# Kernel optimization log

Hardware: AMD Instinct MI355X
Metric: run time of the kernel (lower is better)

The kernel has to match this reference:

```python
import jax, jax.numpy as jnp
import numpy as np

B, SEQ, FEAT, OUT = 8192, 128, 16, 512
D = SEQ * FEAT  # 2048 flattened input dim
H1, H2 = 128, 64


def setup_inputs() -> dict:
    key = jax.random.key(0)
    ks = jax.random.split(key, 9)
    def lin(k, fan_in, shape):
        bound = 1.0 / np.sqrt(fan_in)
        return jax.random.uniform(k, shape, jnp.float32, -bound, bound)
    return {
        "x": jax.random.normal(ks[0], (B, SEQ, FEAT), jnp.float32),
        "W1": lin(ks[1], D, (H1, D)),  "b1": lin(ks[2], D, (H1,)),
        "W2": lin(ks[3], H1, (H2, H1)), "b2": lin(ks[4], H1, (H2,)),
        "W3": lin(ks[5], H2, (D, H2)),  "b3": lin(ks[6], H2, (D,)),
        "Wp": lin(ks[7], D, (OUT, D)),  "bp": lin(ks[8], D, (OUT,)),
    }


def reference(x, W1, b1, W2, b2, W3, b3, Wp, bp):
    # Flatten: [B, D]
    xf = x.reshape(x.shape[0], -1)
    # Forward through base MLP (dropout = identity in eval) to get ReLU masks.
    h1 = xf @ W1.T + b1            # [B, H1]
    m1 = (h1 > 0).astype(xf.dtype)
    h2 = (h1 * m1) @ W2.T + b2     # [B, H2]
    m2 = (h2 > 0).astype(xf.dtype)
    # Per-sample Jacobian of base_forward: J = W3 diag(m2) W2 diag(m1) W1  [D, D]
    # v = (J - J^T) @ 1 = J @ 1 - J^T @ 1 ; both are cheap chained matvecs.
    w1_rows = W1.sum(axis=1)       # W1 @ 1_D, [H1]
    row = ((m1 * w1_rows) @ W2.T * m2) @ W3.T        # J @ 1, [B, D]
    w3_cols = W3.sum(axis=0)       # W3^T @ 1_D, [H2]
    col = ((m2 * w3_cols) @ W2 * m1) @ W1            # J^T @ 1, [B, D]
    v = row - col                  # antisymmetrized row-sum, [B, D]
    return v @ Wp.T + bp           # [B, OUT]
```

## Files before the change

### kernel.cpp

```cpp
#include <hip/hip_runtime.h>


#define B_N   8192
#define D_N   2048
#define H1_N  128
#define H2_N  64
#define OUT_N 512

#define WS_W1R  0
#define WS_W3C  128
#define WS_W2T  256
#define WS_WPC  16384
#define WS_WPCP 114688
#define WS_H1PA 131072
#define WS_H1PB 1179648
#define WS_AT   2228224

__global__ __launch_bounds__(256) void k_pre(const float* __restrict__ W1,
                                             const float* __restrict__ W2,
                                             const float* __restrict__ W3,
                                             float* __restrict__ ws) {
  int b = blockIdx.x, t = threadIdx.x;
  __shared__ float red[256];
  if (b < 128) {
    float s = 0.f;
    const float* row = W1 + (size_t)b * D_N;
    for (int i = t; i < D_N; i += 256) s += row[i];
    red[t] = s; __syncthreads();
    for (int off = 128; off > 0; off >>= 1) { if (t < off) red[t] += red[t + off]; __syncthreads(); }
    if (t == 0) ws[WS_W1R + b] = red[0];
  } else if (b < 192) {
    int c = b - 128;
    float s = 0.f;
    for (int d = t; d < D_N; d += 256) s += W3[(size_t)d * H2_N + c];
    red[t] = s; __syncthreads();
    for (int off = 128; off > 0; off >>= 1) { if (t < off) red[t] += red[t + off]; __syncthreads(); }
    if (t == 0) ws[WS_W3C + c] = red[0];
  } else {
    int flat = (b - 192) * 256 + t;
    int j = flat >> 6, u = flat & 63;
    ws[WS_W2T + j * H2_N + u] = W2[u * H1_N + j];
  }
}

__global__ __launch_bounds__(128) void k_wpc(const float* __restrict__ W1,
                                             const float* __restrict__ W3,
                                             const float* __restrict__ Wp,
                                             float* __restrict__ ws) {
  int b = blockIdx.x, t = threadIdx.x;
  int rt = b % 6, ot = (b / 6) % 8, kc = b / 48;
  __shared__ float As[32 * 68];
  __shared__ float Bs[64 * 68];
  int rg = t >> 4, og = t & 15;
  float acc[4][4];
  #pragma unroll
  for (int i = 0; i < 4; ++i)
    #pragma unroll
    for (int j = 0; j < 4; ++j) acc[i][j] = 0.f;
  for (int sub = 0; sub < 4; ++sub) {
    int k0 = kc * 256 + sub * 64;
    __syncthreads();
    if (rt < 2) {
      #pragma unroll
      for (int i = 0; i < 4; ++i) {
        int flat = i * 128 + t;
        int rq = flat & 7, kl = flat >> 3;
        const float4 v = *reinterpret_cast<const float4*>(W3 + (size_t)(k0 + kl) * H2_N + rt * 32 + rq * 4);
        As[(rq * 4 + 0) * 68 + kl] = v.x;
        As[(rq * 4 + 1) * 68 + kl] = v.y;
        As[(rq * 4 + 2) * 68 + kl] = v.z;
        As[(rq * 4 + 3) * 68 + kl] = v.w;
      }
    } else {
      #pragma unroll
      for (int i = 0; i < 4; ++i) {
        int flat = i * 128 + t;
        int kq = flat & 15, rl = flat >> 4;
        const float4 v = *reinterpret_cast<const float4*>(W1 + (size_t)(rt * 32 + rl - 64) * D_N + k0 + kq * 4);
        *reinterpret_cast<float4*>(&As[rl * 68 + kq * 4]) = v;
      }
    }
    #pragma unroll
    for (int i = 0; i < 8; ++i) {
      int flat = i * 128 + t;
      int kq = flat & 15, ol = flat >> 4;
      const float4 v = *reinterpret_cast<const float4*>(Wp + (size_t)(ot * 64 + ol) * D_N + k0 + kq * 4);
      *reinterpret_cast<float4*>(&Bs[ol * 68 + kq * 4]) = v;
    }
    __syncthreads();
    for (int k = 0; k < 64; k += 4) {
      float4 a[4], bb[4];
      #pragma unroll
      for (int i = 0; i < 4; ++i) a[i] = *reinterpret_cast<const float4*>(&As[(rg * 4 + i) * 68 + k]);
      #pragma unroll
      for (int j = 0; j < 4; ++j) bb[j] = *reinterpret_cast<const float4*>(&Bs[(og * 4 + j) * 68 + k]);
      #pragma unroll
      for (int i = 0; i < 4; ++i)
        #pragma unroll
        for (int j = 0; j < 4; ++j) {
          acc[i][j] = fmaf(a[i].x, bb[j].x, acc[i][j]);
          acc[i][j] = fmaf(a[i].y, bb[j].y, acc[i][j]);
          acc[i][j] = fmaf(a[i].z, bb[j].z, acc[i][j]);
          acc[i][j] = fmaf(a[i].w, bb[j].w, acc[i][j]);
        }
    }
  }
  float* P = ws + WS_WPCP + (size_t)kc * (192 * 512);
  #pragma unroll
  for (int i = 0; i < 4; ++i) {
    int r = rt * 32 + rg * 4 + i;
    #pragma unroll
    for (int j = 0; j < 4; ++j)
      P[r * 512 + ot * 64 + og * 4 + j] = acc[i][j];
  }
}

__global__ __launch_bounds__(256) void k_wpc_red(float* __restrict__ ws) {
  int idx = (blockIdx.x * 256 + threadIdx.x) * 4;
  float4 s = make_float4(0.f, 0.f, 0.f, 0.f);
  #pragma unroll
  for (int p = 0; p < 8; ++p) {
    const float4 v = *reinterpret_cast<const float4*>(ws + WS_WPCP + (size_t)p * (192 * 512) + idx);
    s.x += v.x; s.y += v.y; s.z += v.z; s.w += v.w;
  }
  *reinterpret_cast<float4*>(ws + WS_WPC + idx) = s;
}

__global__ __launch_bounds__(128) void k_h1(const float* __restrict__ x,
                                            const float* __restrict__ W1,
                                            float* __restrict__ ws) {
  __shared__ float xs[64 * 65];
  int b = blockIdx.x;
  int st = b >> 3, ut = (b >> 1) & 3, kh = b & 1;
  int s0 = st * 64;
  int t = threadIdx.x;
  int lane = t & 63;
  int wv = __builtin_amdgcn_readfirstlane(t >> 6);
  int u0 = ut * 32 + wv * 16;
  float acc[16];
  #pragma unroll
  for (int i = 0; i < 16; ++i) acc[i] = 0.f;
  for (int cc = 0; cc < 16; ++cc) {
    int kc = kh * 1024 + cc * 64;
    __syncthreads();
    #pragma unroll
    for (int r = 0; r < 8; ++r) {
      int flat = r * 128 + t;
      int kq = flat & 15;
      int s  = flat >> 4;
      const float4 v = *reinterpret_cast<const float4*>(x + (size_t)(s0 + s) * D_N + kc + kq * 4);
      xs[(kq * 4 + 0) * 65 + s] = v.x;
      xs[(kq * 4 + 1) * 65 + s] = v.y;
      xs[(kq * 4 + 2) * 65 + s] = v.z;
      xs[(kq * 4 + 3) * 65 + s] = v.w;
    }
    __syncthreads();
    const float* wbase = W1 + (size_t)u0 * D_N + kc;
    for (int k4 = 0; k4 < 64; k4 += 4) {
      float a0 = xs[(k4 + 0) * 65 + lane];
      float a1 = xs[(k4 + 1) * 65 + lane];
      float a2 = xs[(k4 + 2) * 65 + lane];
      float a3 = xs[(k4 + 3) * 65 + lane];
      #pragma unroll
      for (int uu = 0; uu < 16; ++uu) {
        const float* wr = wbase + (size_t)uu * D_N + k4;
        float c = acc[uu];
        c = fmaf(wr[0], a0, c);
        c = fmaf(wr[1], a1, c);
        c = fmaf(wr[2], a2, c);
        c = fmaf(wr[3], a3, c);
        acc[uu] = c;
      }
    }
  }
  float* hp = ws + (kh ? WS_H1PB : WS_H1PA);
  #pragma unroll
  for (int uu = 0; uu < 16; ++uu)
    hp[(size_t)(u0 + uu) * B_N + s0 + lane] = acc[uu];
}

__global__ __launch_bounds__(512) void k_mid(const float* __restrict__ b1,
                                             const float* __restrict__ b2,
                                             const float* __restrict__ W2,
                                             float* __restrict__ ws) {
  __shared__ float hs[128 * 65];
  __shared__ float sb[64 * 65];
  int s0 = blockIdx.x * 64;
  int t = threadIdx.x;
  int lane = t & 63;
  int wv = __builtin_amdgcn_readfirstlane(t >> 6);
  const float* PA = ws + WS_H1PA;
  const float* PB = ws + WS_H1PB;
  const float* W2T = ws + WS_W2T;
  const float* w1r = ws + WS_W1R;
  const float* w3c = ws + WS_W3C;
  float* A_T = ws + WS_AT;
  #pragma unroll
  for (int jj = 0; jj < 16; ++jj) {
    int j = wv * 16 + jj;
    hs[j * 65 + lane] = PA[(size_t)j * B_N + s0 + lane]
                      + PB[(size_t)j * B_N + s0 + lane] + b1[j];
  }
  __syncthreads();
  {
    int u0 = wv * 8;
    float h2a[8], ta[8];
    #pragma unroll
    for (int i = 0; i < 8; ++i) { h2a[i] = b2[u0 + i]; ta[i] = 0.f; }
    for (int j = 0; j < H1_N; ++j) {
      float h = hs[j * 65 + lane];
      float g = fmaxf(h, 0.f);
      float a = (h > 0.f) ? w1r[j] : 0.f;
      const float* w2row = W2T + j * H2_N + u0;
      #pragma unroll
      for (int uu = 0; uu < 8; ++uu) {
        h2a[uu] = fmaf(w2row[uu], g, h2a[uu]);
        ta[uu]  = fmaf(w2row[uu], a, ta[uu]);
      }
    }
    #pragma unroll
    for (int uu = 0; uu < 8; ++uu) {
      bool m2 = h2a[uu] > 0.f;
      A_T[(size_t)(u0 + uu) * B_N + s0 + lane] = m2 ? ta[uu] : 0.f;
      sb[(u0 + uu) * 65 + lane] = m2 ? w3c[u0 + uu] : 0.f;
    }
  }
  __syncthreads();
  {
    int j0 = wv * 16;
    float c[16];
    #pragma unroll
    for (int i = 0; i < 16; ++i) c[i] = 0.f;
    for (int u = 0; u < H2_N; ++u) {
      float sv = sb[u * 65 + lane];
      const float* w2row = W2 + u * H1_N + j0;
      #pragma unroll
      for (int jj = 0; jj < 16; ++jj)
        c[jj] = fmaf(w2row[jj], sv, c[jj]);
    }
    #pragma unroll
    for (int jj = 0; jj < 16; ++jj) {
      float h = hs[(j0 + jj) * 65 + lane];
      A_T[(size_t)(64 + j0 + jj) * B_N + s0 + lane] = (h > 0.f) ? -c[jj] : 0.f;
    }
  }
}

__global__ __launch_bounds__(512) void k_out2(const float* __restrict__ bp,
                                              const float* __restrict__ ws,
                                              float* __restrict__ out) {
  __shared__ float wp[192 * 64];
  int b = blockIdx.x;
  int ow = b & 7, st8 = b >> 3;
  int t = threadIdx.x;
  int lane = t & 63;
  int wv = __builtin_amdgcn_readfirstlane(t >> 6);
  int s0 = st8 * 128 + wv * 16;
  int o = ow * 64 + lane;
  const float* Wpc = ws + WS_WPC;
  const float* A_T = ws + WS_AT;
  #pragma unroll
  for (int i = 0; i < 6; ++i) {
    int idx = (i * 512 + t) * 4;
    int k = idx >> 6, ol = idx & 63;
    *reinterpret_cast<float4*>(&wp[idx]) =
        *reinterpret_cast<const float4*>(Wpc + (size_t)k * OUT_N + ow * 64 + ol);
  }
  __syncthreads();
  float acc[16];
  float bpv = bp[o];
  #pragma unroll
  for (int i = 0; i < 16; ++i) acc[i] = bpv;
  for (int k = 0; k < 192; ++k) {
    float wvv = wp[k * 64 + lane];
    const float* arow = A_T + (size_t)k * B_N + s0;
    #pragma unroll
    for (int si = 0; si < 16; ++si)
      acc[si] = fmaf(arow[si], wvv, acc[si]);
  }
  #pragma unroll
  for (int si = 0; si < 16; ++si)
    out[(size_t)(s0 + si) * OUT_N + o] = acc[si];
}

extern "C" void kernel_launch(void* const* d_in, const int* in_sizes, int n_in,
                              void* d_out, int out_size, void* d_ws, size_t ws_size,
                              hipStream_t stream) {
  const float* x  = (const float*)d_in[0];
  const float* W1 = (const float*)d_in[1];
  const float* b1 = (const float*)d_in[2];
  const float* W2 = (const float*)d_in[3];
  const float* b2 = (const float*)d_in[4];
  const float* W3 = (const float*)d_in[5];
  const float* Wp = (const float*)d_in[7];
  const float* bp = (const float*)d_in[8];
  float* out = (float*)d_out;
  float* ws  = (float*)d_ws;

  hipLaunchKernelGGL(k_pre,     dim3(224),  dim3(256), 0, stream, W1, W2, W3, ws);
  hipLaunchKernelGGL(k_wpc,     dim3(384),  dim3(128), 0, stream, W1, W3, Wp, ws);
  hipLaunchKernelGGL(k_wpc_red, dim3(96),   dim3(256), 0, stream, ws);
  hipLaunchKernelGGL(k_h1,      dim3(1024), dim3(128), 0, stream, x, W1, ws);
  hipLaunchKernelGGL(k_mid,     dim3(128),  dim3(512), 0, stream, b1, b2, W2, ws);
  hipLaunchKernelGGL(k_out2,    dim3(512),  dim3(512), 0, stream, bp, ws, out);
}
```

Measured before the change: 313.8 us.

## Split mid-stage kernel into smaller kernels and double k_h1 grid

k_h1 now gives each wave 8 output units instead of 16 and launches twice as many blocks, raising parallelism. The single 128-block k_mid is split into three kernels: one sums the two h1 partials plus bias in place, one computes h2 and the masked term, and one computes the W2-transposed product. Intermediates go through global workspace instead of shared memory. This should fill more of the GPU, at the cost of extra launches and extra global traffic. In k_h1, x is re-read for every unit tile, so doubling the grid doubles those reads.

Result: slower. 324.9 us (+3.6%).

```diff
diff --git a/kernel.cpp b/kernel.cpp
--- a/kernel.cpp
+++ b/kernel.cpp
@@ -14,6 +14,7 @@
 #define WS_WPCP 114688
 #define WS_H1PA 131072
 #define WS_H1PB 1179648
+#define WS_SBT  1179648
 #define WS_AT   2228224
 
 __global__ __launch_bounds__(256) void k_pre(const float* __restrict__ W1,
@@ -131,15 +132,15 @@
                                             float* __restrict__ ws) {
   __shared__ float xs[64 * 65];
   int b = blockIdx.x;
-  int st = b >> 3, ut = (b >> 1) & 3, kh = b & 1;
+  int st = b >> 4, ut = (b >> 1) & 7, kh = b & 1;
   int s0 = st * 64;
   int t = threadIdx.x;
   int lane = t & 63;
   int wv = __builtin_amdgcn_readfirstlane(t >> 6);
-  int u0 = ut * 32 + wv * 16;
-  float acc[16];
-  #pragma unroll
-  for (int i = 0; i < 16; ++i) acc[i] = 0.f;
+  int u0 = ut * 16 + wv * 8;
+  float acc[8];
+  #pragma unroll
+  for (int i = 0; i < 8; ++i) acc[i] = 0.f;
   for (int cc = 0; cc < 16; ++cc) {
     int kc = kh * 1024 + cc * 64;
     __syncthreads();
@@ -162,7 +163,7 @@
       float a2 = xs[(k4 + 2) * 65 + lane];
       float a3 = xs[(k4 + 3) * 65 + lane];
       #pragma unroll
-      for (int uu = 0; uu < 16; ++uu) {
+      for (int uu = 0; uu < 8; ++uu) {
         const float* wr = wbase + (size_t)uu * D_N + k4;
         float c = acc[uu];
         c = fmaf(wr[0], a0, c);
@@ -175,74 +176,88 @@
   }
   float* hp = ws + (kh ? WS_H1PB : WS_H1PA);
   #pragma unroll
-  for (int uu = 0; uu < 16; ++uu)
+  for (int uu = 0; uu < 8; ++uu)
     hp[(size_t)(u0 + uu) * B_N + s0 + lane] = acc[uu];
 }
 
-__global__ __launch_bounds__(512) void k_mid(const float* __restrict__ b1,
-                                             const float* __restrict__ b2,
-                                             const float* __restrict__ W2,
+__global__ __launch_bounds__(256) void k_hsum(const float* __restrict__ b1,
+                                              float* __restrict__ ws) {
+  int idx = (blockIdx.x * 256 + threadIdx.x) * 4;
+  int j = idx >> 13;
+  float bb = b1[j];
+  const float4 pa = *reinterpret_cast<const float4*>(ws + WS_H1PA + idx);
+  const float4 pb = *reinterpret_cast<const float4*>(ws + WS_H1PB + idx);
+  float4 r;
+  r.x = pa.x + pb.x + bb;
+  r.y = pa.y + pb.y + bb;
+  r.z = pa.z + pb.z + bb;
+  r.w = pa.w + pb.w + bb;
+  *reinterpret_cast<float4*>(ws + WS_H1PA + idx) = r;
+}
+
+__global__ __launch_bounds__(128) void k_h2t(const float* __restrict__ b2,
                                              float* __restrict__ ws) {
-  __shared__ float hs[128 * 65];
-  __shared__ float sb[64 * 65];
-  int s0 = blockIdx.x * 64;
+  int b = blockIdx.x;
+  int st = b >> 2, ut = b & 3;
+  int s0 = st * 64;
   int t = threadIdx.x;
   int lane = t & 63;
   int wv = __builtin_amdgcn_readfirstlane(t >> 6);
-  const float* PA = ws + WS_H1PA;
-  const float* PB = ws + WS_H1PB;
+  int u0 = ut * 16 + wv * 8;
+  const float* H1  = ws + WS_H1PA;
   const float* W2T = ws + WS_W2T;
   const float* w1r = ws + WS_W1R;
   const float* w3c = ws + WS_W3C;
+  float h2a[8], ta[8];
+  #pragma unroll
+  for (int i = 0; i < 8; ++i) { h2a[i] = b2[u0 + i]; ta[i] = 0.f; }
+  for (int j = 0; j < H1_N; ++j) {
+    float h = H1[(size_t)j * B_N + s0 + lane];
+    float g = fmaxf(h, 0.f);
+    float a = (h > 0.f) ? w1r[j] : 0.f;
+    const float* w2row = W2T + j * H2_N + u0;
+    #pragma unroll
+    for (int uu = 0; uu < 8; ++uu) {
+      h2a[uu] = fmaf(w2row[uu], g, h2a[uu]);
+      ta[uu]  = fmaf(w2row[uu], a, ta[uu]);
+    }
+  }
   float* A_T = ws + WS_AT;
-  #pragma unroll
-  for (int jj = 0; jj < 16; ++jj) {
-    int j = wv * 16 + jj;
-    hs[j * 65 + lane] = PA[(size_t)j * B_N + s0 + lane]
-                      + PB[(size_t)j * B_N + s0 + lane] + b1[j];
-  }
-  __syncthreads();
-  {
-    int u0 = wv * 8;
-    float h2a[8], ta[8];
-    #pragma unroll
-    for (int i = 0; i < 8; ++i) { h2a[i] = b2[u0 + i]; ta[i] = 0.f; }
-    for (int j = 0; j < H1_N; ++j) {
-      float h = hs[j * 65 + lane];
-      float g = fmaxf(h, 0.f);
-      float a = (h > 0.f) ? w1r[j] : 0.f;
-      const float* w2row = W2T + j * H2_N + u0;
-      #pragma unroll
-      for (int uu = 0; uu < 8; ++uu) {
-        h2a[uu] = fmaf(w2row[uu], g, h2a[uu]);
-        ta[uu]  = fmaf(w2row[uu], a, ta[uu]);
-      }
-    }
-    #pragma unroll
-    for (int uu = 0; uu < 8; ++uu) {
-      bool m2 = h2a[uu] > 0.f;
-      A_T[(size_t)(u0 + uu) * B_N + s0 + lane] = m2 ? ta[uu] : 0.f;
-      sb[(u0 + uu) * 65 + lane] = m2 ? w3c[u0 + uu] : 0.f;
-    }
-  }
-  __syncthreads();
-  {
-    int j0 = wv * 16;
-    float c[16];
-    #pragma unroll
-    for (int i = 0; i < 16; ++i) c[i] = 0.f;
-    for (int u = 0; u < H2_N; ++u) {
-      float sv = sb[u * 65 + lane];
-      const float* w2row = W2 + u * H1_N + j0;
-      #pragma unroll
-      for (int jj = 0; jj < 16; ++jj)
-        c[jj] = fmaf(w2row[jj], sv, c[jj]);
-    }
-    #pragma unroll
-    for (int jj = 0; jj < 16; ++jj) {
-      float h = hs[(j0 + jj) * 65 + lane];
-      A_T[(size_t)(64 + j0 + jj) * B_N + s0 + lane] = (h > 0.f) ? -c[jj] : 0.f;
-    }
+  float* SBT = ws + WS_SBT;
+  #pragma unroll
+  for (int uu = 0; uu < 8; ++uu) {
+    bool m2 = h2a[uu] > 0.f;
+    A_T[(size_t)(u0 + uu) * B_N + s0 + lane] = m2 ? ta[uu] : 0.f;
+    SBT[(size_t)(u0 + uu) * B_N + s0 + lane] = m2 ? w3c[u0 + uu] : 0.f;
+  }
+}
+
+__global__ __launch_bounds__(128) void k_c1(const float* __restrict__ W2,
+                                            float* __restrict__ ws) {
+  int b = blockIdx.x;
+  int st = b >> 3, jt = b & 7;
+  int s0 = st * 64;
+  int t = threadIdx.x;
+  int lane = t & 63;
+  int wv = __builtin_amdgcn_readfirstlane(t >> 6);
+  int j0 = jt * 16 + wv * 8;
+  const float* H1  = ws + WS_H1PA;
+  const float* SBT = ws + WS_SBT;
+  float c[8];
+  #pragma unroll
+  for (int i = 0; i < 8; ++i) c[i] = 0.f;
+  for (int u = 0; u < H2_N; ++u) {
+    float sv = SBT[(size_t)u * B_N + s0 + lane];
+    const float* w2row = W2 + u * H1_N + j0;
+    #pragma unroll
+    for (int jj = 0; jj < 8; ++jj)
+      c[jj] = fmaf(w2row[jj], sv, c[jj]);
+  }
+  float* A_T = ws + WS_AT;
+  #pragma unroll
+  for (int jj = 0; jj < 8; ++jj) {
+    float h = H1[(size_t)(j0 + jj) * B_N + s0 + lane];
+    A_T[(size_t)(64 + j0 + jj) * B_N + s0 + lane] = (h > 0.f) ? -c[jj] : 0.f;
   }
 }
 
@@ -300,7 +315,9 @@
   hipLaunchKernelGGL(k_pre,     dim3(224),  dim3(256), 0, stream, W1, W2, W3, ws);
   hipLaunchKernelGGL(k_wpc,     dim3(384),  dim3(128), 0, stream, W1, W3, Wp, ws);
   hipLaunchKernelGGL(k_wpc_red, dim3(96),   dim3(256), 0, stream, ws);
-  hipLaunchKernelGGL(k_h1,      dim3(1024), dim3(128), 0, stream, x, W1, ws);
-  hipLaunchKernelGGL(k_mid,     dim3(128),  dim3(512), 0, stream, b1, b2, W2, ws);
+  hipLaunchKernelGGL(k_h1,      dim3(2048), dim3(128), 0, stream, x, W1, ws);
+  hipLaunchKernelGGL(k_hsum,    dim3(1024), dim3(256), 0, stream, b1, ws);
+  hipLaunchKernelGGL(k_h2t,     dim3(512),  dim3(128), 0, stream, b2, ws);
+  hipLaunchKernelGGL(k_c1,      dim3(1024), dim3(128), 0, stream, W2, ws);
   hipLaunchKernelGGL(k_out2,    dim3(512),  dim3(512), 0, stream, bp, ws, out);
 }
```
